# Performance work log

Measured on AMD Instinct MI355X. Metric: run time of the kernel, lower is better.

The kernel has to match this reference:

```python
import jax, jax.numpy as jnp
import numpy as np

HEADS = 8
DIM_HEAD = 64
SCALE = DIM_HEAD ** -0.5


def setup_inputs() -> dict:
    key = jax.random.key(0)
    ks = jax.random.split(key, 6)
    B, T, C, H, W = 16, 64, 512, 64, 64
    inner = HEADS * DIM_HEAD  # 512
    return {
        "vision_feature": jax.random.normal(ks[0], (B, C, H, W), jnp.float32),
        "language_feature": jax.random.normal(ks[1], (B, T, C), jnp.float32),
        "mask": jnp.ones((B, T), jnp.int32),  # unused by the module's forward
        "Wq": jax.random.normal(ks[2], (inner, C), jnp.float32) * (C ** -0.5),
        "Wk": jax.random.normal(ks[3], (inner, C), jnp.float32) * (C ** -0.5),
        "Wv": jax.random.normal(ks[4], (inner, C), jnp.float32) * (C ** -0.5),
        "Wo": jax.random.normal(ks[5], (C, inner), jnp.float32) * (inner ** -0.5),
    }


def reference(vision_feature, language_feature, mask, Wq, Wk, Wv, Wo):
    B, T, C = language_feature.shape
    _, _, H, W = vision_feature.shape
    S = H * W
    # 1x1 conv projections == matmuls over the channel dim
    q = jnp.einsum('btc,ic->bti', language_feature, Wq)           # (B, T, inner)
    vis = vision_feature.reshape(B, C, S)                          # (B, C, S)
    k = jnp.einsum('ic,bcs->bis', Wk, vis)                         # (B, inner, S)
    v = jnp.einsum('ic,bcs->bis', Wv, vis)                         # (B, inner, S)
    # split heads: channel index = n*dim_head + d  (n outermost)
    q = q.reshape(B, T, HEADS, DIM_HEAD).transpose(2, 0, 1, 3)     # (h, B, T, d)
    k = k.reshape(B, HEADS, DIM_HEAD, S).transpose(1, 0, 2, 3)     # (h, B, d, S)
    v = v.reshape(B, HEADS, DIM_HEAD, S).transpose(1, 0, 3, 2)     # (h, B, S, d)
    att = jax.nn.softmax(jnp.einsum('hbtd,hbds->hbts', q, k) * SCALE, axis=-1)
    out = jnp.einsum('hbts,hbsd->hbtd', att, v)                    # (h, B, T, d)
    # merge heads back: b (n c) tokens -> equivalently (B, T, h*d)
    out = out.transpose(1, 2, 0, 3).reshape(B, T, HEADS * DIM_HEAD)
    out = jnp.einsum('bti,oi->bto', out, Wo)                       # (B, T, C)
    return out
```

## Files before the change

### kernel.cpp

```cpp
#include <hip/hip_runtime.h>
#include <stdint.h>

typedef __attribute__((ext_vector_type(8))) short short8;
typedef __attribute__((ext_vector_type(4))) short short4v;
typedef __attribute__((ext_vector_type(4))) float float4v;
typedef __attribute__((ext_vector_type(8))) __bf16 bf16x8;

#define NCH 4

__device__ __forceinline__ float4v mfma16x16x32(short8 a, short8 b, float4v c) {
  return __builtin_amdgcn_mfma_f32_16x16x32_bf16(
      __builtin_bit_cast(bf16x8, a), __builtin_bit_cast(bf16x8, b), c, 0, 0, 0);
}

__device__ __forceinline__ short f2bf(float f) {
  uint32_t u = __builtin_bit_cast(uint32_t, f);
  u += 0x7fffu + ((u >> 16) & 1u);
  return (short)(u >> 16);
}

__device__ __forceinline__ float bf2f(short s) {
  return __builtin_bit_cast(float, ((uint32_t)(uint16_t)s) << 16);
}

__device__ __forceinline__ void load_lds16(const short* g, short* l) {
  __builtin_amdgcn_global_load_lds(
      (const __attribute__((address_space(1))) void*)g,
      (__attribute__((address_space(3))) void*)l, 16, 0, 0);
}

__global__ __launch_bounds__(256) void convert5(
    const float* __restrict__ sl, short* __restrict__ dl,
    const float* __restrict__ s1, short* __restrict__ d1,
    const float* __restrict__ s2, short* __restrict__ d2,
    const float* __restrict__ s3, short* __restrict__ d3,
    const float* __restrict__ s4, short* __restrict__ d4) {
  const float* src; short* dst; int n4;
  switch (blockIdx.y) {
    case 0: src = sl; dst = dl; n4 = 131072; break;
    case 1: src = s1; dst = d1; n4 = 65536; break;
    case 2: src = s2; dst = d2; n4 = 65536; break;
    case 3: src = s3; dst = d3; n4 = 65536; break;
    default: src = s4; dst = d4; n4 = 65536; break;
  }
  const int stride = gridDim.x * blockDim.x;
  for (int i = blockIdx.x * blockDim.x + threadIdx.x; i < n4; i += stride) {
    float4v v = *(const float4v*)(src + (long)i * 4);
    short4v o;
#pragma unroll
    for (int r = 0; r < 4; r++) o[r] = f2bf(v[r]);
    *(short4v*)(dst + (long)i * 4) = o;
  }
}

template <int OUT_F32>
__global__ __launch_bounds__(256) void gemm_nt(
    const short* __restrict__ A, const short* __restrict__ B,
    void* __restrict__ C, int K, int ldc, float scale) {
  __shared__ alignas(16) short lA[128 * 32];
  __shared__ alignas(16) short lB[128 * 32];
  const int tid = threadIdx.x;
  const int lane = tid & 63, w = tid >> 6;
  const int quad = lane >> 4, l16 = lane & 15;
  const int wm = w >> 1, wn = w & 1;
  const long m0 = (long)blockIdx.y * 128, n0 = (long)blockIdx.x * 128;

  float4v acc[4][4];
#pragma unroll
  for (int i = 0; i < 4; i++)
#pragma unroll
    for (int j = 0; j < 4; j++) acc[i][j] = (float4v)0.0f;

  const int srow = tid >> 2;
  const int scol = (((tid & 3) ^ ((srow >> 1) & 3))) * 8;

  for (int kt = 0; kt < K; kt += 32) {
    load_lds16(&A[(m0 + srow) * K + kt + scol], &lA[tid * 8]);
    load_lds16(&A[(m0 + 64 + srow) * K + kt + scol], &lA[2048 + tid * 8]);
    load_lds16(&B[(n0 + srow) * K + kt + scol], &lB[tid * 8]);
    load_lds16(&B[(n0 + 64 + srow) * K + kt + scol], &lB[2048 + tid * 8]);
    __syncthreads();

    short8 af[4], bf[4];
#pragma unroll
    for (int t = 0; t < 4; t++) {
      const int ra = wm * 64 + t * 16 + l16;
      const int rb = wn * 64 + t * 16 + l16;
      af[t] = *(const short8*)&lA[ra * 32 + ((quad ^ ((ra >> 1) & 3)) * 8)];
      bf[t] = *(const short8*)&lB[rb * 32 + ((quad ^ ((rb >> 1) & 3)) * 8)];
    }
#pragma unroll
    for (int i = 0; i < 4; i++)
#pragma unroll
      for (int j = 0; j < 4; j++)
        acc[i][j] = mfma16x16x32(af[i], bf[j], acc[i][j]);
    __syncthreads();
  }

  const int cm = wm * 64 + quad * 4;
  const int cn = wn * 64 + l16;
  if (OUT_F32) {
    float* Cf = (float*)C;
#pragma unroll
    for (int i = 0; i < 4; i++)
#pragma unroll
      for (int j = 0; j < 4; j++) {
        const long gn = n0 + cn + j * 16;
#pragma unroll
        for (int r = 0; r < 4; r++)
          Cf[(m0 + cm + i * 16 + r) * (long)ldc + gn] = acc[i][j][r] * scale;
      }
  } else {
    short* Cs = (short*)C;
#pragma unroll
    for (int i = 0; i < 4; i++)
#pragma unroll
      for (int j = 0; j < 4; j++) {
        const long gn = n0 + cn + j * 16;
#pragma unroll
        for (int r = 0; r < 4; r++)
          Cs[(m0 + cm + i * 16 + r) * (long)ldc + gn] = f2bf(acc[i][j][r] * scale);
      }
  }
}

__global__ __launch_bounds__(512) void gemm_kv(
    const short* __restrict__ Wk, const short* __restrict__ Wv,
    const short* __restrict__ visT, long sV,
    short* __restrict__ kout, short* __restrict__ vout, long sKV) {
  __shared__ alignas(16) short smem[12288];
  short* lWk = smem;
  short* lWv = smem + 4096;
  short* lVis = smem + 8192;
  const int tid = threadIdx.x;
  const int lane = tid & 63, w = tid >> 6;
  const int quad = lane >> 4, l16 = lane & 15;
  const int role = w >> 2;
  const int wq = w & 3, wm = wq >> 1, wn = wq & 1;
  const long n0 = (long)blockIdx.x * 128;
  const long m0 = (long)blockIdx.y * 128;
  const short* vis = visT + blockIdx.z * sV;
  short* kz = kout + blockIdx.z * sKV;
  short* vz = vout + blockIdx.z * sKV;

  float4v acc[4][4];
#pragma unroll
  for (int i = 0; i < 4; i++)
#pragma unroll
    for (int j = 0; j < 4; j++) acc[i][j] = (float4v)0.0f;

  const int srow = tid >> 2;
  const int scol = (((tid & 3) ^ ((srow >> 1) & 3))) * 8;
  const short* lW = role ? lWv : lWk;

  for (int kt = 0; kt < 512; kt += 32) {
    load_lds16(&Wk[(m0 + srow) * 512 + kt + scol], &lWk[tid * 8]);
    load_lds16(&Wv[(m0 + srow) * 512 + kt + scol], &lWv[tid * 8]);
    load_lds16(&vis[(n0 + srow) * 512 + kt + scol], &lVis[tid * 8]);
    __syncthreads();

    short8 af[4], bf[4];
#pragma unroll
    for (int t = 0; t < 4; t++) {
      const int ra = wm * 64 + t * 16 + l16;
      const int rb = wn * 64 + t * 16 + l16;
      af[t] = *(const short8*)&lW[ra * 32 + ((quad ^ ((ra >> 1) & 3)) * 8)];
      bf[t] = *(const short8*)&lVis[rb * 32 + ((quad ^ ((rb >> 1) & 3)) * 8)];
    }
#pragma unroll
    for (int i = 0; i < 4; i++)
#pragma unroll
      for (int j = 0; j < 4; j++)
        acc[i][j] = mfma16x16x32(af[i], bf[j], acc[i][j]);
    __syncthreads();
  }

  const int cm = wm * 64 + quad * 4;
  const int cn = wn * 64 + l16;

  if (role == 1) {
#pragma unroll
    for (int i = 0; i < 4; i++)
#pragma unroll
      for (int j = 0; j < 4; j++) {
        const long gn = n0 + cn + j * 16;
#pragma unroll
        for (int r = 0; r < 4; r++)
          vz[(m0 + cm + i * 16 + r) * 4096 + gn] = f2bf(acc[i][j][r]);
      }
  }

  short* scratch = smem;
#pragma unroll
  for (int h = 0; h < 2; h++) {
    __syncthreads();
    if (role == 0 && wn == h) {
#pragma unroll
      for (int j = 0; j < 4; j++)
#pragma unroll
        for (int i = 0; i < 4; i++) {
          const int nloc = j * 16 + l16;
          const int m = wm * 64 + i * 16 + quad * 4;
          short4v pk;
#pragma unroll
          for (int r = 0; r < 4; r++) pk[r] = f2bf(acc[i][j][r]);
          *(short4v*)&scratch[nloc * 136 + m] = pk;
        }
    }
    __syncthreads();
    {
      const int row = tid >> 3;
      const int off = (tid & 7) * 16;
      short8 v0 = *(const short8*)&scratch[row * 136 + off];
      short8 v1 = *(const short8*)&scratch[row * 136 + off + 8];
      *(short8*)&kz[(n0 + h * 64 + row) * 512 + m0 + off] = v0;
      *(short8*)&kz[(n0 + h * 64 + row) * 512 + m0 + off + 8] = v1;
    }
  }
}

__global__ __launch_bounds__(256) void transpose_f2b(
    const float* __restrict__ vis, short* __restrict__ visT) {
  __shared__ alignas(16) short buf[64][68];
  const int tid = threadIdx.x;
  const long bz = blockIdx.z;
  const long s0 = (long)blockIdx.x * 64;
  const long c0 = (long)blockIdx.y * 64;
  const float* src = vis + bz * 512 * 4096;
  short* dst = visT + bz * 4096 * 512;
  const int tr = tid >> 4;
  const int tc4 = (tid & 15) * 4;
#pragma unroll
  for (int i = 0; i < 4; i++) {
    const int c = tr + i * 16;
    float4v val = *(const float4v*)&src[(c0 + c) * 4096 + s0 + tc4];
    buf[tc4 + 0][c] = f2bf(val[0]);
    buf[tc4 + 1][c] = f2bf(val[1]);
    buf[tc4 + 2][c] = f2bf(val[2]);
    buf[tc4 + 3][c] = f2bf(val[3]);
  }
  __syncthreads();
#pragma unroll
  for (int i = 0; i < 4; i++) {
    const int s = tr + i * 16;
    short4v val = *(const short4v*)&buf[s][tc4];
    *(short4v*)&dst[(s0 + s) * 512 + c0 + tc4] = val;
  }
}

__global__ __launch_bounds__(256) void attn_part(
    const short* __restrict__ q, const short* __restrict__ kws,
    const short* __restrict__ vws, float* __restrict__ Opart,
    float* __restrict__ lpart, int b0) {
  const int h = blockIdx.x;
  const int bz = blockIdx.y;
  const int ch = blockIdx.z;
  const int tid = threadIdx.x;
  const int lane = tid & 63, w = tid >> 6;
  const int quad = lane >> 4, l16 = lane & 15;

  __shared__ alignas(16) short lq[64 * 64];
  __shared__ alignas(16) short lk[128 * 64];
  __shared__ alignas(16) short lv[64 * 128];
  __shared__ alignas(16) short lp[64 * 128];
  __shared__ float lsum[64];

  const short* qb = q + ((long)(b0 + bz) * 64) * 512 + h * 64;
  const short* kb = kws + (long)bz * 4096 * 512 + h * 64;
  const short* vb = vws + (long)bz * 512 * 4096 + (long)h * 64 * 4096;

  if (tid < 64) lsum[tid] = 0.0f;
  {
    const int qr = tid >> 3;
    const int qc = ((tid & 7) ^ (qr & 7)) * 8;
    load_lds16(&qb[qr * 512 + qc], &lq[tid * 8]);
    load_lds16(&qb[(32 + qr) * 512 + qc], &lq[2048 + tid * 8]);
  }
  __syncthreads();

  short8 aq[4][2];
#pragma unroll
  for (int mt = 0; mt < 4; mt++)
#pragma unroll
    for (int ks = 0; ks < 2; ks++) {
      const int ra = mt * 16 + l16;
      aq[mt][ks] = *(const short8*)&lq[ra * 64 + (((ks * 4 + quad) ^ (ra & 7)) * 8)];
    }

  float4v osc[4];
#pragma unroll
  for (int mt = 0; mt < 4; mt++) osc[mt] = (float4v)0.0f;
  float lrow[4][4] = {};

  const int send = ch * (4096 / NCH) + (4096 / NCH);
  for (int s0 = ch * (4096 / NCH); s0 < send; s0 += 128) {
#pragma unroll
    for (int it = 0; it < 4; it++) {
      const int li = tid + it * 256;
      const int kr = li >> 3;
      const int kc = ((li & 7) ^ (kr & 7)) * 8;
      load_lds16(&kb[(long)(s0 + kr) * 512 + kc], &lk[li * 8]);
    }
#pragma unroll
    for (int it = 0; it < 4; it++) {
      const int li = tid + it * 256;
      const int vr = li >> 4;
      const int vc = ((li & 15) ^ (vr & 7)) * 8;
      load_lds16(&vb[(long)vr * 4096 + s0 + vc], &lv[li * 8]);
    }
    __syncthreads();

    float4v sc[4][2];
#pragma unroll
    for (int mt = 0; mt < 4; mt++)
#pragma unroll
      for (int jn = 0; jn < 2; jn++) sc[mt][jn] = (float4v)0.0f;
#pragma unroll
    for (int ks = 0; ks < 2; ks++) {
      short8 bk[2];
#pragma unroll
      for (int jn = 0; jn < 2; jn++) {
        const int rb = (2 * w + jn) * 16 + l16;
        bk[jn] = *(const short8*)&lk[rb * 64 + (((ks * 4 + quad) ^ (rb & 7)) * 8)];
      }
#pragma unroll
      for (int mt = 0; mt < 4; mt++)
#pragma unroll
        for (int jn = 0; jn < 2; jn++)
          sc[mt][jn] = mfma16x16x32(aq[mt][ks], bk[jn], sc[mt][jn]);
    }

#pragma unroll
    for (int mt = 0; mt < 4; mt++)
#pragma unroll
      for (int jn = 0; jn < 2; jn++)
#pragma unroll
        for (int r = 0; r < 4; r++) {
          const float scv = fminf(fmaxf(sc[mt][jn][r], -80.0f), 30.0f);
          const short sp = f2bf(__expf(scv));
          lrow[mt][r] += bf2f(sp);
          const int rowp = mt * 16 + quad * 4 + r;
          const int col = (2 * w + jn) * 16 + l16;
          lp[rowp * 128 + (((col >> 3) ^ (rowp & 7)) * 8) + (col & 7)] = sp;
        }
    __syncthreads();

#pragma unroll
    for (int ks = 0; ks < 4; ks++) {
      const int rv = w * 16 + l16;
      const short8 bv = *(const short8*)&lv[rv * 128 + (((ks * 4 + quad) ^ (rv & 7)) * 8)];
#pragma unroll
      for (int mt = 0; mt < 4; mt++) {
        const int rp = mt * 16 + l16;
        const short8 ap = *(const short8*)&lp[rp * 128 + (((ks * 4 + quad) ^ (rp & 7)) * 8)];
        osc[mt] = mfma16x16x32(ap, bv, osc[mt]);
      }
    }
    __syncthreads();
  }

#pragma unroll
  for (int mt = 0; mt < 4; mt++)
#pragma unroll
    for (int r = 0; r < 4; r++) {
      float v = lrow[mt][r];
      v += __shfl_xor(v, 1);
      v += __shfl_xor(v, 2);
      v += __shfl_xor(v, 4);
      v += __shfl_xor(v, 8);
      if (l16 == 0) atomicAdd(&lsum[mt * 16 + quad * 4 + r], v);
    }
  __syncthreads();

  const long bh = bz * 8 + h;
  float* op = Opart + ((bh * NCH + ch) * 64) * 64 + w * 16 + l16;
#pragma unroll
  for (int mt = 0; mt < 4; mt++)
#pragma unroll
    for (int r = 0; r < 4; r++)
      op[(long)(mt * 16 + quad * 4 + r) * 64] = osc[mt][r];
  if (tid < 64) lpart[(bh * NCH + ch) * 64 + tid] = lsum[tid];
}

__global__ __launch_bounds__(256) void attn_combine(
    const float* __restrict__ Opart, const float* __restrict__ lpart,
    short* __restrict__ tmp, int b0, int nbh) {
  const int total = nbh * 4096;
  for (int idx = blockIdx.x * 256 + threadIdx.x; idx < total;
       idx += gridDim.x * 256) {
    const int bh = idx >> 12;
    const int td = idx & 4095;
    const int t = td >> 6, d = td & 63;
    float o = 0.0f, l = 0.0f;
#pragma unroll
    for (int c = 0; c < NCH; c++) {
      o += Opart[((long)bh * NCH + c) * 4096 + td];
      l += lpart[(bh * NCH + c) * 64 + t];
    }
    const int b = b0 + (bh >> 3), h = bh & 7;
    tmp[((long)b * 64 + t) * 512 + h * 64 + d] = f2bf(o / l);
  }
}

extern "C" void kernel_launch(void* const* d_in, const int* in_sizes, int n_in,
                              void* d_out, int out_size, void* d_ws, size_t ws_size,
                              hipStream_t stream) {
  (void)in_sizes; (void)n_in; (void)out_size;
  const float* vis = (const float*)d_in[0];
  const float* lang = (const float*)d_in[1];
  const float* Wq = (const float*)d_in[3];
  const float* Wk = (const float*)d_in[4];
  const float* Wv = (const float*)d_in[5];
  const float* Wo = (const float*)d_in[6];
  float* out = (float*)d_out;

  char* ws = (char*)d_ws;
  const size_t MB = 1 << 20;
  short* q_ws = (short*)(ws + 0 * MB);
  short* tmp_ws = (short*)(ws + 1 * MB);
  short* langb = (short*)(ws + 2 * MB);
  short* Wqb = (short*)(ws + 3 * MB);
  short* Wkb = (short*)(ws + 3 * MB + 512 * 1024);
  short* Wvb = (short*)(ws + 4 * MB);
  short* Wob = (short*)(ws + 4 * MB + 512 * 1024);
  char* grp = ws + 5 * MB;

  const long batch_elems = 4096l * 512;
  int g = 16;
  const int cands[5] = {1, 2, 4, 8, 16};
  for (int ci = 0; ci < 5; ci++) {
    const size_t need = 5 * MB + 3ull * (16 / cands[ci]) * batch_elems * 2;
    if (need <= ws_size) { g = cands[ci]; break; }
  }
  const int Bg = 16 / g;
  short* visT = (short*)grp;
  short* k_ws = visT + (long)Bg * batch_elems;
  short* v_ws = k_ws + (long)Bg * batch_elems;
  float* Opart = (float*)visT;
  float* lptr = Opart + (long)Bg * 8 * NCH * 4096;

  convert5<<<dim3(128, 5), 256, 0, stream>>>(lang, langb, Wq, Wqb, Wk, Wkb,
                                             Wv, Wvb, Wo, Wob);

  gemm_nt<0><<<dim3(4, 8), 256, 0, stream>>>(langb, Wqb, q_ws, 512, 512, 0.125f);

  for (int gi = 0; gi < g; gi++) {
    const int b0 = gi * Bg;
    transpose_f2b<<<dim3(64, 8, Bg), 256, 0, stream>>>(vis + (long)b0 * batch_elems, visT);
    gemm_kv<<<dim3(32, 4, Bg), 512, 0, stream>>>(Wkb, Wvb, visT, batch_elems,
                                                 k_ws, v_ws, batch_elems);
    attn_part<<<dim3(8, Bg, NCH), 256, 0, stream>>>(q_ws, k_ws, v_ws, Opart, lptr, b0);
    attn_combine<<<512, 256, 0, stream>>>(Opart, lptr, tmp_ws, b0, Bg * 8);
  }

  gemm_nt<1><<<dim3(4, 8), 256, 0, stream>>>(tmp_ws, Wob, out, 512, 512, 1.0f);
}
```

Before: 389.3 us.

## Prefetch next K/V and GEMM tiles into LDS while computing current tile

In the GEMM, the KV-projection and the attention kernels, operands of the current tile are now read from LDS into registers first. The next tile's global-to-LDS load is then issued before the MFMA work, so memory latency overlaps compute instead of being exposed at each loop head. The same single LDS buffer is reused, with a barrier after the fragment reads. This raises register pressure (extra bk/bv fragments held) and can lower occupancy. It also relies on the async LDS loads completing before the next barrier.

```diff
diff --git a/kernel.cpp b/kernel.cpp
--- a/kernel.cpp
+++ b/kernel.cpp
@@ -74,11 +74,12 @@
   const int srow = tid >> 2;
   const int scol = (((tid & 3) ^ ((srow >> 1) & 3))) * 8;
 
+  load_lds16(&A[(m0 + srow) * K + scol], &lA[tid * 8]);
+  load_lds16(&A[(m0 + 64 + srow) * K + scol], &lA[2048 + tid * 8]);
+  load_lds16(&B[(n0 + srow) * K + scol], &lB[tid * 8]);
+  load_lds16(&B[(n0 + 64 + srow) * K + scol], &lB[2048 + tid * 8]);
+
   for (int kt = 0; kt < K; kt += 32) {
-    load_lds16(&A[(m0 + srow) * K + kt + scol], &lA[tid * 8]);
-    load_lds16(&A[(m0 + 64 + srow) * K + kt + scol], &lA[2048 + tid * 8]);
-    load_lds16(&B[(n0 + srow) * K + kt + scol], &lB[tid * 8]);
-    load_lds16(&B[(n0 + 64 + srow) * K + kt + scol], &lB[2048 + tid * 8]);
     __syncthreads();
 
     short8 af[4], bf[4];
@@ -89,12 +90,19 @@
       af[t] = *(const short8*)&lA[ra * 32 + ((quad ^ ((ra >> 1) & 3)) * 8)];
       bf[t] = *(const short8*)&lB[rb * 32 + ((quad ^ ((rb >> 1) & 3)) * 8)];
     }
+    __syncthreads();
+
+    if (kt + 32 < K) {
+      load_lds16(&A[(m0 + srow) * K + kt + 32 + scol], &lA[tid * 8]);
+      load_lds16(&A[(m0 + 64 + srow) * K + kt + 32 + scol], &lA[2048 + tid * 8]);
+      load_lds16(&B[(n0 + srow) * K + kt + 32 + scol], &lB[tid * 8]);
+      load_lds16(&B[(n0 + 64 + srow) * K + kt + 32 + scol], &lB[2048 + tid * 8]);
+    }
 #pragma unroll
     for (int i = 0; i < 4; i++)
 #pragma unroll
       for (int j = 0; j < 4; j++)
         acc[i][j] = mfma16x16x32(af[i], bf[j], acc[i][j]);
-    __syncthreads();
   }
 
   const int cm = wm * 64 + quad * 4;
@@ -153,10 +161,11 @@
   const int scol = (((tid & 3) ^ ((srow >> 1) & 3))) * 8;
   const short* lW = role ? lWv : lWk;
 
+  load_lds16(&Wk[(m0 + srow) * 512 + scol], &lWk[tid * 8]);
+  load_lds16(&Wv[(m0 + srow) * 512 + scol], &lWv[tid * 8]);
+  load_lds16(&vis[(n0 + srow) * 512 + scol], &lVis[tid * 8]);
+
   for (int kt = 0; kt < 512; kt += 32) {
-    load_lds16(&Wk[(m0 + srow) * 512 + kt + scol], &lWk[tid * 8]);
-    load_lds16(&Wv[(m0 + srow) * 512 + kt + scol], &lWv[tid * 8]);
-    load_lds16(&vis[(n0 + srow) * 512 + kt + scol], &lVis[tid * 8]);
     __syncthreads();
 
     short8 af[4], bf[4];
@@ -167,12 +176,18 @@
       af[t] = *(const short8*)&lW[ra * 32 + ((quad ^ ((ra >> 1) & 3)) * 8)];
       bf[t] = *(const short8*)&lVis[rb * 32 + ((quad ^ ((rb >> 1) & 3)) * 8)];
     }
+    __syncthreads();
+
+    if (kt + 32 < 512) {
+      load_lds16(&Wk[(m0 + srow) * 512 + kt + 32 + scol], &lWk[tid * 8]);
+      load_lds16(&Wv[(m0 + srow) * 512 + kt + 32 + scol], &lWv[tid * 8]);
+      load_lds16(&vis[(n0 + srow) * 512 + kt + 32 + scol], &lVis[tid * 8]);
+    }
 #pragma unroll
     for (int i = 0; i < 4; i++)
 #pragma unroll
       for (int j = 0; j < 4; j++)
         acc[i][j] = mfma16x16x32(af[i], bf[j], acc[i][j]);
-    __syncthreads();
   }
 
   const int cm = wm * 64 + quad * 4;
@@ -276,6 +291,22 @@
     load_lds16(&qb[qr * 512 + qc], &lq[tid * 8]);
     load_lds16(&qb[(32 + qr) * 512 + qc], &lq[2048 + tid * 8]);
   }
+  const int s0_first = ch * (4096 / NCH);
+  const int send = s0_first + (4096 / NCH);
+#pragma unroll
+  for (int it = 0; it < 4; it++) {
+    const int li = tid + it * 256;
+    const int kr = li >> 3;
+    const int kc = ((li & 7) ^ (kr & 7)) * 8;
+    load_lds16(&kb[(long)(s0_first + kr) * 512 + kc], &lk[li * 8]);
+  }
+#pragma unroll
+  for (int it = 0; it < 4; it++) {
+    const int li = tid + it * 256;
+    const int vr = li >> 4;
+    const int vc = ((li & 15) ^ (vr & 7)) * 8;
+    load_lds16(&vb[(long)vr * 4096 + s0_first + vc], &lv[li * 8]);
+  }
   __syncthreads();
 
   short8 aq[4][2];
@@ -292,43 +323,52 @@
   for (int mt = 0; mt < 4; mt++) osc[mt] = (float4v)0.0f;
   float lrow[4][4] = {};
 
-  const int send = ch * (4096 / NCH) + (4096 / NCH);
-  for (int s0 = ch * (4096 / NCH); s0 < send; s0 += 128) {
-#pragma unroll
-    for (int it = 0; it < 4; it++) {
-      const int li = tid + it * 256;
-      const int kr = li >> 3;
-      const int kc = ((li & 7) ^ (kr & 7)) * 8;
-      load_lds16(&kb[(long)(s0 + kr) * 512 + kc], &lk[li * 8]);
-    }
-#pragma unroll
-    for (int it = 0; it < 4; it++) {
-      const int li = tid + it * 256;
-      const int vr = li >> 4;
-      const int vc = ((li & 15) ^ (vr & 7)) * 8;
-      load_lds16(&vb[(long)vr * 4096 + s0 + vc], &lv[li * 8]);
-    }
-    __syncthreads();
-
-    float4v sc[4][2];
-#pragma unroll
-    for (int mt = 0; mt < 4; mt++)
-#pragma unroll
-      for (int jn = 0; jn < 2; jn++) sc[mt][jn] = (float4v)0.0f;
-#pragma unroll
-    for (int ks = 0; ks < 2; ks++) {
-      short8 bk[2];
+  for (int s0 = s0_first; s0 < send; s0 += 128) {
+    short8 bk[2][2];
+#pragma unroll
+    for (int ks = 0; ks < 2; ks++)
 #pragma unroll
       for (int jn = 0; jn < 2; jn++) {
         const int rb = (2 * w + jn) * 16 + l16;
-        bk[jn] = *(const short8*)&lk[rb * 64 + (((ks * 4 + quad) ^ (rb & 7)) * 8)];
-      }
+        bk[ks][jn] = *(const short8*)&lk[rb * 64 + (((ks * 4 + quad) ^ (rb & 7)) * 8)];
+      }
+    short8 bv[4];
+#pragma unroll
+    for (int ks = 0; ks < 4; ks++) {
+      const int rv = w * 16 + l16;
+      bv[ks] = *(const short8*)&lv[rv * 128 + (((ks * 4 + quad) ^ (rv & 7)) * 8)];
+    }
+    __syncthreads();
+
+    if (s0 + 128 < send) {
+#pragma unroll
+      for (int it = 0; it < 4; it++) {
+        const int li = tid + it * 256;
+        const int kr = li >> 3;
+        const int kc = ((li & 7) ^ (kr & 7)) * 8;
+        load_lds16(&kb[(long)(s0 + 128 + kr) * 512 + kc], &lk[li * 8]);
+      }
+#pragma unroll
+      for (int it = 0; it < 4; it++) {
+        const int li = tid + it * 256;
+        const int vr = li >> 4;
+        const int vc = ((li & 15) ^ (vr & 7)) * 8;
+        load_lds16(&vb[(long)vr * 4096 + s0 + 128 + vc], &lv[li * 8]);
+      }
+    }
+
+    float4v sc[4][2];
+#pragma unroll
+    for (int mt = 0; mt < 4; mt++)
+#pragma unroll
+      for (int jn = 0; jn < 2; jn++) sc[mt][jn] = (float4v)0.0f;
+#pragma unroll
+    for (int ks = 0; ks < 2; ks++)
 #pragma unroll
       for (int mt = 0; mt < 4; mt++)
 #pragma unroll
         for (int jn = 0; jn < 2; jn++)
-          sc[mt][jn] = mfma16x16x32(aq[mt][ks], bk[jn], sc[mt][jn]);
-    }
+          sc[mt][jn] = mfma16x16x32(aq[mt][ks], bk[ks][jn], sc[mt][jn]);
 
 #pragma unroll
     for (int mt = 0; mt < 4; mt++)
@@ -346,16 +386,13 @@
     __syncthreads();
 
 #pragma unroll
-    for (int ks = 0; ks < 4; ks++) {
-      const int rv = w * 16 + l16;
-      const short8 bv = *(const short8*)&lv[rv * 128 + (((ks * 4 + quad) ^ (rv & 7)) * 8)];
+    for (int ks = 0; ks < 4; ks++)
 #pragma unroll
       for (int mt = 0; mt < 4; mt++) {
         const int rp = mt * 16 + l16;
         const short8 ap = *(const short8*)&lp[rp * 128 + (((ks * 4 + quad) ^ (rp & 7)) * 8)];
-        osc[mt] = mfma16x16x32(ap, bv, osc[mt]);
-      }
-    }
+        osc[mt] = mfma16x16x32(ap, bv[ks], osc[mt]);
+      }
     __syncthreads();
   }
 
```

Result: faster. 379.7 us (-2.5%).
